# Kernel optimization log

Hardware: AMD Instinct MI355X
Metric: run time of the kernel (lower is better)

Reference implementation:

```python
import jax, jax.numpy as jnp
import numpy as np

# ---- model constants (match init_kwargs) ----
E = 128; GH = 8; GD = E // GH; GL = 3          # graph emb / heads / layers
SH = 4; SD = E // SH; SL = 4                   # sequence transformer
ATOM = 64; BOND = 16; RBF_K = 32; CUTOFF = 5.0
VOCAB = 64; SEQL = 128
N = 32                                          # nodes per graph (equal-size graphs)
GC = 64; GS = 16; BMOL = 16; DEG = 64; GF = 3   # conf graphs / scaffold graphs / molecules / edges-per-graph
LN_EPS = 1e-5
CENTERS = jnp.linspace(0.0, CUTOFF, RBF_K)
GAMMA = (CUTOFF / (RBF_K - 1)) ** -2            # GaussianRBF gamma = (center spacing)^-2


def _ln(x, g, b):
    mu = x.mean(-1, keepdims=True)
    var = ((x - mu) ** 2).mean(-1, keepdims=True)
    return (x - mu) / jnp.sqrt(var + LN_EPS) * g + b


def _graph_encoder(x, edge_index, edge_attr, pos, G, p):
    # node projection
    h = x @ p["gproj_w"] + p["gproj_b"]                      # [G*N, E]
    # edge features: bond features + RBF(distance)
    d = jnp.clip(edge_attr[:, -1], 0.0, 10.0)
    rbf = jnp.exp(-GAMMA * (d[:, None] - CENTERS) ** 2)       # [M, K]
    ef = jnp.concatenate([edge_attr[:, :-1], rbf], axis=1)    # [M, BOND+K]
    # EdgeNetwork: per-edge matrix (gather -> matvec -> scatter-add)
    M = ef.shape[0]
    m = (ef @ p["elin_w"] + p["elin_b"]).reshape(M, E, E)
    msg = jnp.einsum("mef,mf->me", m, h[edge_index[1]])      # [M, E]
    aggr = jnp.zeros_like(h).at[edge_index[0]].add(msg)
    h = _ln(h + aggr, p["eln_g"], p["eln_b"])
    # dense per-graph layout (equal-size graphs -> reshape, mask is all-true)
    hb = h.reshape(G, N, E)
    pp = pos.reshape(G, N, 3)
    d2 = jnp.sum((pp[:, :, None, :] - pp[:, None, :, :]) ** 2, axis=-1)
    dist = jnp.where(d2 > 0, jnp.sqrt(jnp.where(d2 > 0, d2, 1.0)), 0.0)  # safe cdist
    inv_sqrt_d = 1.0 / np.sqrt(GD)
    for l in range(GL):
        def heads(t):
            return t.reshape(G, N, GH, GD).transpose(0, 2, 1, 3)
        q = heads(hb @ p["gt_qw"][l] + p["gt_qb"][l])
        k = heads(hb @ p["gt_kw"][l] + p["gt_kb"][l])
        v = heads(hb @ p["gt_vw"][l] + p["gt_vb"][l])
        s = jnp.einsum("bhnd,bhmd->bhnm", q, k) * inv_sqrt_d + dist[:, None]
        s = jnp.clip(s, -10.0, 10.0)
        a = jax.nn.softmax(s, axis=-1)                       # all nodes valid -> no mask
        o = jnp.einsum("bhnm,bhmd->bhnd", a, v).transpose(0, 2, 1, 3).reshape(G, N, E)
        o = o @ p["gt_ow"][l] + p["gt_ob"][l]
        x1 = _ln(hb + o, p["gt_ln1g"][l], p["gt_ln1b"][l])
        ff = jax.nn.relu(x1 @ p["gt_f1w"][l] + p["gt_f1b"][l]) @ p["gt_f2w"][l] + p["gt_f2b"][l]
        hb = _ln(x1 + ff, p["gt_ln2g"][l], p["gt_ln2b"][l])
    # masked mean pool with the source's eps in the denominator
    return hb.sum(1) / (N + 1e-8)


def _seq_encoder(tokens, p):
    B, L = tokens.shape
    x = p["tok_emb"][tokens] + p["pos_emb"][:L][None]        # [B, L, E]
    inv_sqrt_d = 1.0 / np.sqrt(SD)
    for l in range(SL):
        qkv = x @ p["se_inw"][l] + p["se_inb"][l]            # [B, L, 3E]
        q, k, v = jnp.split(qkv, 3, axis=-1)
        def heads(t):
            return t.reshape(B, L, SH, SD).transpose(0, 2, 1, 3)
        q, k, v = heads(q), heads(k), heads(v)
        a = jax.nn.softmax(jnp.einsum("bhnd,bhmd->bhnm", q, k) * inv_sqrt_d, axis=-1)
        o = jnp.einsum("bhnm,bhmd->bhnd", a, v).transpose(0, 2, 1, 3).reshape(B, L, E)
        o = o @ p["se_ow"][l] + p["se_ob"][l]
        x = _ln(x + o, p["se_ln1g"][l], p["se_ln1b"][l])      # post-norm (torch default)
        ff = jax.nn.relu(x @ p["se_f1w"][l] + p["se_f1b"][l]) @ p["se_f2w"][l] + p["se_f2b"][l]
        x = _ln(x + ff, p["se_ln2g"][l], p["se_ln2b"][l])
    return x.mean(1)                                          # [B, E]


def _forward(p, conf_edge_index, scaf_edge_index, tokens, conf_per_mol):
    g_all = _graph_encoder(p["conf_x"], conf_edge_index, p["conf_edge_attr"], p["conf_pos"], GC, p)
    conf_emb = g_all.reshape(-1, conf_per_mol, E).mean(1)     # per-molecule conformer mean (equal counts)
    scaf_emb = _graph_encoder(p["scaf_x"], scaf_edge_index, p["scaf_edge_attr"], p["scaf_pos"], GS, p)
    total = conf_emb + scaf_emb
    seq = _seq_encoder(tokens, p)
    # FusionGating
    gate_h = jax.nn.relu(jnp.concatenate([total, seq], -1) @ p["fg1_w"] + p["fg1_b"])
    gate = jax.nn.sigmoid(gate_h @ p["fg2_w"] + p["fg2_b"])
    fused = gate * total + (1.0 - gate) * seq
    # CrossModalAttention: MHA over a length-1 sequence (unsqueeze(0)) -> softmax
    # weights are identically 1, so attn(q_in, kv, kv) == out_proj(v_proj(kv)).
    g, s = fused, fused
    for l in range(2):
        g2s = (s @ p["cm_g2s_vw"][l] + p["cm_g2s_vb"][l]) @ p["cm_g2s_ow"][l] + p["cm_g2s_ob"][l]
        g = _ln(g + g2s, p["cm_n1g"][l], p["cm_n1b"][l])
        s2g = (g @ p["cm_s2g_vw"][l] + p["cm_s2g_vb"][l]) @ p["cm_s2g_ow"][l] + p["cm_s2g_ob"][l]
        s = _ln(s + s2g, p["cm_n2g"][l], p["cm_n2b"][l])
    final = (g + s) * 0.5
    comb = jnp.concatenate([final, p["graph_features"]], -1)
    return (jax.nn.relu(comb @ p["r1_w"] + p["r1_b"]) @ p["r2_w"] + p["r2_b"])[:, 0]


def setup_inputs() -> dict:
    ks = iter(jax.random.split(jax.random.key(0), 64))
    def nrm(shape, s):
        return (jax.random.normal(next(ks), shape) * s).astype(jnp.float32)
    inp = {}
    def mk_graph(prefix, G):
        inp[prefix + "_x"] = nrm((G * N, ATOM), 1.0)
        off = (jnp.arange(G) * N)[:, None]
        src = jax.random.randint(next(ks), (G, DEG), 0, N) + off   # within-graph edges
        dst = jax.random.randint(next(ks), (G, DEG), 0, N) + off
        inp[prefix + "_edge_index"] = jnp.stack([src.ravel(), dst.ravel()]).astype(jnp.int32)
        bond = jax.random.uniform(next(ks), (G * DEG, BOND))
        dist = jax.random.uniform(next(ks), (G * DEG, 1), minval=0.5, maxval=CUTOFF)
        inp[prefix + "_edge_attr"] = jnp.concatenate([bond, dist], 1).astype(jnp.float32)
        inp[prefix + "_pos"] = nrm((G * N, 3), 2.0)
    mk_graph("conf", GC)
    mk_graph("scaf", GS)
    inp["tokens"] = jax.random.randint(next(ks), (BMOL, SEQL), 1, VOCAB).astype(jnp.int32)
    inp["graph_features"] = nrm((BMOL, GF), 1.0)
    inp["conf_per_mol"] = GC // BMOL
    W = 0.05
    inp["gproj_w"] = nrm((ATOM, E), W); inp["gproj_b"] = jnp.zeros(E)
    inp["elin_w"] = nrm((BOND + RBF_K, E * E), W); inp["elin_b"] = jnp.zeros(E * E)
    inp["eln_g"] = jnp.ones(E); inp["eln_b"] = jnp.zeros(E)
    for nm in ["qw", "kw", "vw", "ow"]:
        inp["gt_" + nm] = nrm((GL, E, E), W)
        inp["gt_" + nm[0] + "b"] = jnp.zeros((GL, E))
    inp["gt_ln1g"] = jnp.ones((GL, E)); inp["gt_ln1b"] = jnp.zeros((GL, E))
    inp["gt_f1w"] = nrm((GL, E, 2 * E), W); inp["gt_f1b"] = jnp.zeros((GL, 2 * E))
    inp["gt_f2w"] = nrm((GL, 2 * E, E), W); inp["gt_f2b"] = jnp.zeros((GL, E))
    inp["gt_ln2g"] = jnp.ones((GL, E)); inp["gt_ln2b"] = jnp.zeros((GL, E))
    inp["tok_emb"] = nrm((VOCAB, E), 0.02); inp["pos_emb"] = nrm((256, E), 0.02)
    inp["se_inw"] = nrm((SL, E, 3 * E), W); inp["se_inb"] = jnp.zeros((SL, 3 * E))
    inp["se_ow"] = nrm((SL, E, E), W); inp["se_ob"] = jnp.zeros((SL, E))
    inp["se_ln1g"] = jnp.ones((SL, E)); inp["se_ln1b"] = jnp.zeros((SL, E))
    inp["se_f1w"] = nrm((SL, E, 2 * E), W); inp["se_f1b"] = jnp.zeros((SL, 2 * E))
    inp["se_f2w"] = nrm((SL, 2 * E, E), W); inp["se_f2b"] = jnp.zeros((SL, E))
    inp["se_ln2g"] = jnp.ones((SL, E)); inp["se_ln2b"] = jnp.zeros((SL, E))
    inp["fg1_w"] = nrm((2 * E, 64), W); inp["fg1_b"] = jnp.zeros(64)
    inp["fg2_w"] = nrm((64, E), W); inp["fg2_b"] = jnp.zeros(E)
    for nm in ["g2s", "s2g"]:
        inp["cm_" + nm + "_vw"] = nrm((2, E, E), W); inp["cm_" + nm + "_vb"] = jnp.zeros((2, E))
        inp["cm_" + nm + "_ow"] = nrm((2, E, E), W); inp["cm_" + nm + "_ob"] = jnp.zeros((2, E))
    inp["cm_n1g"] = jnp.ones((2, E)); inp["cm_n1b"] = jnp.zeros((2, E))
    inp["cm_n2g"] = jnp.ones((2, E)); inp["cm_n2b"] = jnp.zeros((2, E))
    inp["r1_w"] = nrm((E + GF, E), W); inp["r1_b"] = jnp.zeros(E)
    inp["r2_w"] = nrm((E, 1), W); inp["r2_b"] = jnp.zeros(1)
    return inp


def reference(conf_x, conf_edge_attr, conf_pos, scaf_x, scaf_edge_attr, scaf_pos, graph_features,
              gproj_w, gproj_b, elin_w, elin_b, eln_g, eln_b,
              gt_qw, gt_qb, gt_kw, gt_kb, gt_vw, gt_vb, gt_ow, gt_ob,
              gt_ln1g, gt_ln1b, gt_f1w, gt_f1b, gt_f2w, gt_f2b, gt_ln2g, gt_ln2b,
              tok_emb, pos_emb,
              se_inw, se_inb, se_ow, se_ob, se_ln1g, se_ln1b, se_f1w, se_f1b, se_f2w, se_f2b, se_ln2g, se_ln2b,
              fg1_w, fg1_b, fg2_w, fg2_b,
              cm_g2s_vw, cm_g2s_vb, cm_g2s_ow, cm_g2s_ob, cm_n1g, cm_n1b,
              cm_s2g_vw, cm_s2g_vb, cm_s2g_ow, cm_s2g_ob, cm_n2g, cm_n2b,
              r1_w, r1_b, r2_w, r2_b,
              conf_edge_index, scaf_edge_index, tokens, conf_per_mol):
    p = dict(locals())
    return _forward(p, conf_edge_index, scaf_edge_index, tokens, conf_per_mol)
```

## Files before the change

### kernel.cpp

```cpp
#include <hip/hip_runtime.h>
#include <hip/hip_bf16.h>


__device__ __forceinline__ float blk_norm(float v, int e, float* sred)
{
  float s = v;
  #pragma unroll
  for (int o = 1; o < 64; o <<= 1) s += __shfl_xor(s, o);
  if ((e & 63) == 0) sred[e >> 6] = s;
  __syncthreads();
  float mean = (sred[0] + sred[1]) * (1.0f / 128.0f);
  __syncthreads();
  float d = v - mean;
  float s2 = d * d;
  #pragma unroll
  for (int o = 1; o < 64; o <<= 1) s2 += __shfl_xor(s2, o);
  if ((e & 63) == 0) sred[e >> 6] = s2;
  __syncthreads();
  float var = (sred[0] + sred[1]) * (1.0f / 128.0f);
  __syncthreads();
  return d / sqrtf(var + 1e-5f);
}

__global__ __launch_bounds__(128) void node_proj_k(
    const float* __restrict__ cx, const float* __restrict__ sx,
    const float* __restrict__ w, const float* __restrict__ b,
    float* __restrict__ h, float* __restrict__ aggr)
{
  int r = blockIdx.x, e = threadIdx.x;
  const float* x = (r < 2048) ? (cx + (size_t)r * 64) : (sx + (size_t)(r - 2048) * 64);
  __shared__ float xs[64];
  if (e < 64) xs[e] = x[e];
  __syncthreads();
  float acc = b[e];
  for (int a = 0; a < 64; a++) acc += xs[a] * w[a * 128 + e];
  h[(size_t)r * 128 + e] = acc;
  aggr[(size_t)r * 128 + e] = 0.0f;
}

__global__ __launch_bounds__(256) void dist_k(
    const float* __restrict__ cpos, const float* __restrict__ spos, float* __restrict__ dist)
{
  int g = blockIdx.x, tid = threadIdx.x;
  __shared__ float P[96];
  const float* p = (g < 64) ? (cpos + (size_t)g * 96) : (spos + (size_t)(g - 64) * 96);
  if (tid < 96) P[tid] = p[tid];
  __syncthreads();
  #pragma unroll
  for (int jj = 0; jj < 4; jj++) {
    int idx = tid * 4 + jj;
    int i = idx >> 5, j = idx & 31;
    float dx = P[i * 3 + 0] - P[j * 3 + 0];
    float dy = P[i * 3 + 1] - P[j * 3 + 1];
    float dz = P[i * 3 + 2] - P[j * 3 + 2];
    float d2 = dx * dx + dy * dy + dz * dz;
    dist[(size_t)g * 1024 + idx] = (d2 > 0.0f) ? sqrtf(d2) : 0.0f;
  }
}

__global__ __launch_bounds__(256) void edge_gemm_k(
    const float* __restrict__ cea, const float* __restrict__ sea,
    const int* __restrict__ cei, const int* __restrict__ sei,
    const float* __restrict__ h,
    const float* __restrict__ elw, const float* __restrict__ elb,
    float* __restrict__ aggr)
{
  __shared__ float efs[32][8];
  __shared__ float As[32][36];
  __shared__ float Bs[32][136];
  const int tid = threadIdx.x;
  const int m0 = blockIdx.x * 32;
  const int kt0 = blockIdx.y * 28;
  const int c0 = kt0 >> 2;
  {
    int t = tid >> 3, cc = tid & 7;
    if (cc < 7) {
      int c = c0 + cc;
      int m = m0 + t;
      const float* attr = (m < 4096) ? (cea + (size_t)m * 17) : (sea + (size_t)(m - 4096) * 17);
      float val;
      if (c < 16) val = attr[c];
      else if (c < 48) {
        float d = fminf(fmaxf(attr[16], 0.0f), 10.0f);
        float t2 = d - (float)((c - 16) * (5.0 / 31.0));
        val = expf(-38.44f * t2 * t2);
      } else val = 1.0f;
      efs[t][cc] = val;
    }
  }
  const int gk = tid & 31, gt = (tid >> 5) * 4;
  float hreg[4][4];
  #pragma unroll
  for (int i = 0; i < 4; i++) {
    int m = m0 + gt + i;
    int dst = (m < 4096) ? cei[4096 + m] : (sei[1024 + (m - 4096)] + 2048);
    const float* hp = h + (size_t)dst * 128 + gk;
    hreg[i][0] = hp[0]; hreg[i][1] = hp[32]; hreg[i][2] = hp[64]; hreg[i][3] = hp[96];
  }
  const int tn = tid & 31, tm = tid >> 5;
  const int e0 = 4 * tn, t0 = 4 * tm;
  const int se = tid >> 1, sk = (tid & 1) * 16;
  float acc[4][4] = {};
  __syncthreads();
  #pragma unroll 1
  for (int kt = kt0; kt < kt0 + 28; kt++) {
    int c = kt >> 2, cc = c - c0, j = kt & 3;
    float4 av;
    av.x = efs[gt + 0][cc] * hreg[0][j];
    av.y = efs[gt + 1][cc] * hreg[1][j];
    av.z = efs[gt + 2][cc] * hreg[2][j];
    av.w = efs[gt + 3][cc] * hreg[3][j];
    *(float4*)&As[gk][gt] = av;
    const float* bp = ((c < 48) ? (elw + (size_t)c * 16384) : elb) + (size_t)se * 128 + j * 32 + sk;
    float4 w0 = *(const float4*)(bp + 0);
    float4 w1 = *(const float4*)(bp + 4);
    float4 w2 = *(const float4*)(bp + 8);
    float4 w3 = *(const float4*)(bp + 12);
    Bs[sk + 0][se] = w0.x;  Bs[sk + 1][se] = w0.y;  Bs[sk + 2][se] = w0.z;  Bs[sk + 3][se] = w0.w;
    Bs[sk + 4][se] = w1.x;  Bs[sk + 5][se] = w1.y;  Bs[sk + 6][se] = w1.z;  Bs[sk + 7][se] = w1.w;
    Bs[sk + 8][se] = w2.x;  Bs[sk + 9][se] = w2.y;  Bs[sk + 10][se] = w2.z; Bs[sk + 11][se] = w2.w;
    Bs[sk + 12][se] = w3.x; Bs[sk + 13][se] = w3.y; Bs[sk + 14][se] = w3.z; Bs[sk + 15][se] = w3.w;
    __syncthreads();
    #pragma unroll
    for (int kk = 0; kk < 32; kk++) {
      float4 a = *(const float4*)&As[kk][t0];
      float4 b = *(const float4*)&Bs[kk][e0];
      acc[0][0] += a.x * b.x; acc[0][1] += a.x * b.y; acc[0][2] += a.x * b.z; acc[0][3] += a.x * b.w;
      acc[1][0] += a.y * b.x; acc[1][1] += a.y * b.y; acc[1][2] += a.y * b.z; acc[1][3] += a.y * b.w;
      acc[2][0] += a.z * b.x; acc[2][1] += a.z * b.y; acc[2][2] += a.z * b.z; acc[2][3] += a.z * b.w;
      acc[3][0] += a.w * b.x; acc[3][1] += a.w * b.y; acc[3][2] += a.w * b.z; acc[3][3] += a.w * b.w;
    }
    __syncthreads();
  }
  #pragma unroll
  for (int i = 0; i < 4; i++) {
    int m = m0 + t0 + i;
    int src = (m < 4096) ? cei[m] : (sei[m - 4096] + 2048);
    float* dst = aggr + (size_t)src * 128 + e0;
    atomicAdd(dst + 0, acc[i][0]);
    atomicAdd(dst + 1, acc[i][1]);
    atomicAdd(dst + 2, acc[i][2]);
    atomicAdd(dst + 3, acc[i][3]);
  }
}

__device__ __forceinline__ void gemm16_body(
    const float* __restrict__ A, const float* __restrict__ Bp,
    const float* __restrict__ biasp, float* __restrict__ Cp,
    int row0, int ldb, int ldc)
{
  __shared__ float Sa[32][20];
  __shared__ float Bs[32][136];
  const int tid = threadIdx.x;
  const int tm = tid >> 5, tn = tid & 31;
  const int t0 = 2 * tm, e0 = 4 * tn;
  const int ar = tid >> 4, ak = (tid & 15) * 2;
  const int bk = tid >> 3, be = (tid & 7) * 16;
  float acc[2][4] = {};
  for (int k0 = 0; k0 < 128; k0 += 32) {
    float2 av = *(const float2*)(A + (size_t)(row0 + ar) * 128 + k0 + ak);
    Sa[ak][ar] = av.x; Sa[ak + 1][ar] = av.y;
    const float* bp = Bp + (size_t)(k0 + bk) * ldb + be;
    float4 b0v = *(const float4*)(bp + 0);
    float4 b1v = *(const float4*)(bp + 4);
    float4 b2v = *(const float4*)(bp + 8);
    float4 b3v = *(const float4*)(bp + 12);
    Bs[bk][be + 0] = b0v.x;  Bs[bk][be + 1] = b0v.y;  Bs[bk][be + 2] = b0v.z;  Bs[bk][be + 3] = b0v.w;
    Bs[bk][be + 4] = b1v.x;  Bs[bk][be + 5] = b1v.y;  Bs[bk][be + 6] = b1v.z;  Bs[bk][be + 7] = b1v.w;
    Bs[bk][be + 8] = b2v.x;  Bs[bk][be + 9] = b2v.y;  Bs[bk][be + 10] = b2v.z; Bs[bk][be + 11] = b2v.w;
    Bs[bk][be + 12] = b3v.x; Bs[bk][be + 13] = b3v.y; Bs[bk][be + 14] = b3v.z; Bs[bk][be + 15] = b3v.w;
    __syncthreads();
    #pragma unroll
    for (int kk = 0; kk < 32; kk++) {
      float2 a = *(const float2*)&Sa[kk][t0];
      float4 b = *(const float4*)&Bs[kk][e0];
      acc[0][0] += a.x * b.x; acc[0][1] += a.x * b.y; acc[0][2] += a.x * b.z; acc[0][3] += a.x * b.w;
      acc[1][0] += a.y * b.x; acc[1][1] += a.y * b.y; acc[1][2] += a.y * b.z; acc[1][3] += a.y * b.w;
    }
    __syncthreads();
  }
  #pragma unroll
  for (int i = 0; i < 2; i++) {
    float* cp = Cp + (size_t)(row0 + t0 + i) * ldc + e0;
    #pragma unroll
    for (int j = 0; j < 4; j++) cp[j] = acc[i][j] + biasp[e0 + j];
  }
}

__global__ __launch_bounds__(256) void qkv_k(
    int gBlocks,
    const float* __restrict__ ghb,
    const float* gqw, const float* gkw, const float* gvw,
    const float* gqb, const float* gkb, const float* gvb, float* gout,
    const float* __restrict__ sxs, const float* sw, const float* sb, float* sout)
{
  int bx = blockIdx.x;
  if (bx < gBlocks) {
    int z = bx / 160, rt = bx % 160;
    const float* B = (z == 0) ? gqw : (z == 1) ? gkw : gvw;
    const float* bias = (z == 0) ? gqb : (z == 1) ? gkb : gvb;
    gemm16_body(ghb, B, bias, gout + (size_t)z * 327680, rt * 16, 128, 128);
  } else {
    int i = bx - gBlocks;
    int z = i >> 7, rt = i & 127;
    gemm16_body(sxs, sw + z * 128, sb + z * 128, sout + z * 128, rt * 16, 384, 384);
  }
}

__device__ __forceinline__ void gattn_body(
    int g, int h, const float* __restrict__ q, const float* __restrict__ k,
    const float* __restrict__ v, const float* __restrict__ dist, float* __restrict__ o)
{
  __shared__ float qs[32][17], ksh[32][17], vsh[32][17], ss[32][33], rs[32];
  const int tid = threadIdx.x;
  {
    int idx = tid * 2;
    int i = idx >> 4, d = idx & 15;
    size_t base = ((size_t)(g * 32 + i)) * 128 + h * 16 + d;
    qs[i][d] = q[base];  qs[i][d + 1] = q[base + 1];
    ksh[i][d] = k[base]; ksh[i][d + 1] = k[base + 1];
    vsh[i][d] = v[base]; vsh[i][d + 1] = v[base + 1];
  }
  __syncthreads();
  {
    int i = tid >> 3, j0 = (tid & 7) * 4;
    for (int j = j0; j < j0 + 4; j++) {
      float a = 0;
      #pragma unroll
      for (int d = 0; d < 16; d++) a += qs[i][d] * ksh[j][d];
      a = a * 0.25f + dist[(size_t)g * 1024 + i * 32 + j];
      ss[i][j] = fminf(fmaxf(a, -10.0f), 10.0f);
    }
  }
  __syncthreads();
  if (tid < 32) {
    float m = -1e30f;
    for (int j = 0; j < 32; j++) m = fmaxf(m, ss[tid][j]);
    float sm = 0;
    for (int j = 0; j < 32; j++) { float ex = expf(ss[tid][j] - m); ss[tid][j] = ex; sm += ex; }
    rs[tid] = 1.0f / sm;
  }
  __syncthreads();
  {
    int idx = tid * 2;
    int i = idx >> 4, d = idx & 15;
    float a0 = 0, a1 = 0;
    for (int j = 0; j < 32; j++) { float wj = ss[i][j]; a0 += wj * vsh[j][d]; a1 += wj * vsh[j][d + 1]; }
    float r = rs[i];
    size_t base = ((size_t)(g * 32 + i)) * 128 + h * 16 + d;
    o[base] = a0 * r; o[base + 1] = a1 * r;
  }
}

__device__ __forceinline__ void sattn_body(
    int b, int h, int qt, const float* __restrict__ qkv, float* __restrict__ o)
{
  __shared__ float ks[128][33];
  __shared__ float vs[128][33];
  __shared__ float qs2[32][33];
  __shared__ float ss2[32][129];
  __shared__ float red[32][8];
  __shared__ float red2[32][8];
  const int tid = threadIdx.x;
  {
    int l = tid >> 1, d0 = (tid & 1) * 16;
    const float* kp = qkv + ((size_t)(b * 128 + l)) * 384 + 128 + h * 32 + d0;
    #pragma unroll
    for (int j = 0; j < 16; j++) { ks[l][d0 + j] = kp[j]; vs[l][d0 + j] = kp[128 + j]; }
  }
  {
    int i = tid >> 3, d0 = (tid & 7) * 4;
    const float* qp = qkv + ((size_t)(b * 128 + qt * 32 + i)) * 384 + h * 32 + d0;
    #pragma unroll
    for (int j = 0; j < 4; j++) qs2[i][d0 + j] = qp[j];
  }
  __syncthreads();
  const int i = tid >> 3, sub = tid & 7;
  {
    int j0 = sub * 16;
    for (int j = j0; j < j0 + 16; j++) {
      float a = 0;
      #pragma unroll
      for (int d = 0; d < 32; d++) a += qs2[i][d] * ks[j][d];
      ss2[i][j] = a * 0.17677669529663687f;
    }
  }
  __syncthreads();
  float m = -1e30f;
  for (int j = sub; j < 128; j += 8) m = fmaxf(m, ss2[i][j]);
  red[i][sub] = m;
  __syncthreads();
  float mm = red[i][0];
  #pragma unroll
  for (int t = 1; t < 8; t++) mm = fmaxf(mm, red[i][t]);
  float ps = 0;
  for (int j = sub; j < 128; j += 8) { float ex = expf(ss2[i][j] - mm); ss2[i][j] = ex; ps += ex; }
  red2[i][sub] = ps;
  __syncthreads();
  float sm = 0;
  #pragma unroll
  for (int t = 0; t < 8; t++) sm += red2[i][t];
  float rinv = 1.0f / sm;
  {
    int d0 = sub * 4;
    float a0 = 0, a1 = 0, a2 = 0, a3 = 0;
    for (int j = 0; j < 128; j++) {
      float wj = ss2[i][j];
      a0 += wj * vs[j][d0 + 0]; a1 += wj * vs[j][d0 + 1];
      a2 += wj * vs[j][d0 + 2]; a3 += wj * vs[j][d0 + 3];
    }
    float* op = o + ((size_t)(b * 128 + qt * 32 + i)) * 128 + h * 32 + d0;
    op[0] = a0 * rinv; op[1] = a1 * rinv; op[2] = a2 * rinv; op[3] = a3 * rinv;
  }
}

__global__ __launch_bounds__(256) void attn_k(
    int gBlocks, const float* q, const float* k, const float* v,
    const float* dist, float* go, const float* qkv, float* so)
{
  int bx = blockIdx.x;
  if (bx < gBlocks) gattn_body(bx >> 3, bx & 7, q, k, v, dist, go);
  else { int i = bx - gBlocks; sattn_body(i >> 4, (i >> 2) & 3, i & 3, qkv, so); }
}

__device__ __forceinline__ void tail_body(
    int row0, const float* __restrict__ A,
    const float* __restrict__ Wo, const float* __restrict__ bo, const float* __restrict__ res,
    const float* __restrict__ g1, const float* __restrict__ b1n,
    const float* __restrict__ W1, const float* __restrict__ b1f,
    const float* __restrict__ W2, const float* __restrict__ b2f,
    const float* __restrict__ g2, const float* __restrict__ b2n,
    float* __restrict__ Out)
{
  __shared__ float x1[16][132];
  __shared__ float hid[16][260];
  __shared__ __align__(16) float sbuf[4352];
  __shared__ float Sa[32][20];
  float (*BsA)[136] = (float(*)[136])sbuf;
  float (*Bs1)[260] = (float(*)[260])sbuf;
  float (*Bs2)[136] = (float(*)[136])sbuf;
  const int tid = threadIdx.x;
  {
    const int tm = tid >> 5, tn = tid & 31;
    const int t0 = 2 * tm, e0 = 4 * tn;
    const int ar = tid >> 4, ak = (tid & 15) * 2;
    const int bk = tid >> 3, be = (tid & 7) * 16;
    float acc[2][4] = {};
    for (int k0 = 0; k0 < 128; k0 += 32) {
      float2 av = *(const float2*)(A + (size_t)(row0 + ar) * 128 + k0 + ak);
      Sa[ak][ar] = av.x; Sa[ak + 1][ar] = av.y;
      const float* bp = Wo + (size_t)(k0 + bk) * 128 + be;
      float4 b0v = *(const float4*)(bp + 0);
      float4 b1v = *(const float4*)(bp + 4);
      float4 b2v = *(const float4*)(bp + 8);
      float4 b3v = *(const float4*)(bp + 12);
      BsA[bk][be + 0] = b0v.x;  BsA[bk][be + 1] = b0v.y;  BsA[bk][be + 2] = b0v.z;  BsA[bk][be + 3] = b0v.w;
      BsA[bk][be + 4] = b1v.x;  BsA[bk][be + 5] = b1v.y;  BsA[bk][be + 6] = b1v.z;  BsA[bk][be + 7] = b1v.w;
      BsA[bk][be + 8] = b2v.x;  BsA[bk][be + 9] = b2v.y;  BsA[bk][be + 10] = b2v.z; BsA[bk][be + 11] = b2v.w;
      BsA[bk][be + 12] = b3v.x; BsA[bk][be + 13] = b3v.y; BsA[bk][be + 14] = b3v.z; BsA[bk][be + 15] = b3v.w;
      __syncthreads();
      #pragma unroll
      for (int kk = 0; kk < 32; kk++) {
        float2 a = *(const float2*)&Sa[kk][t0];
        float4 b = *(const float4*)&BsA[kk][e0];
        acc[0][0] += a.x * b.x; acc[0][1] += a.x * b.y; acc[0][2] += a.x * b.z; acc[0][3] += a.x * b.w;
        acc[1][0] += a.y * b.x; acc[1][1] += a.y * b.y; acc[1][2] += a.y * b.z; acc[1][3] += a.y * b.w;
      }
      __syncthreads();
    }
    #pragma unroll
    for (int i = 0; i < 2; i++) {
      int r = row0 + t0 + i;
      float v0 = acc[i][0] + bo[e0 + 0] + res[(size_t)r * 128 + e0 + 0];
      float v1 = acc[i][1] + bo[e0 + 1] + res[(size_t)r * 128 + e0 + 1];
      float v2 = acc[i][2] + bo[e0 + 2] + res[(size_t)r * 128 + e0 + 2];
      float v3 = acc[i][3] + bo[e0 + 3] + res[(size_t)r * 128 + e0 + 3];
      float s = v0 + v1 + v2 + v3;
      #pragma unroll
      for (int o = 1; o < 32; o <<= 1) s += __shfl_xor(s, o);
      float mean = s * (1.0f / 128.0f);
      float d0 = v0 - mean, d1 = v1 - mean, d2 = v2 - mean, d3 = v3 - mean;
      float sq = d0 * d0 + d1 * d1 + d2 * d2 + d3 * d3;
      #pragma unroll
      for (int o = 1; o < 32; o <<= 1) sq += __shfl_xor(sq, o);
      float rstd = 1.0f / sqrtf(sq * (1.0f / 128.0f) + 1e-5f);
      x1[t0 + i][e0 + 0] = d0 * rstd * g1[e0 + 0] + b1n[e0 + 0];
      x1[t0 + i][e0 + 1] = d1 * rstd * g1[e0 + 1] + b1n[e0 + 1];
      x1[t0 + i][e0 + 2] = d2 * rstd * g1[e0 + 2] + b1n[e0 + 2];
      x1[t0 + i][e0 + 3] = d3 * rstd * g1[e0 + 3] + b1n[e0 + 3];
    }
  }
  __syncthreads();
  {
    const int tm = tid >> 6, tn = tid & 63;
    const int t0 = 4 * tm, e0 = 4 * tn;
    const int ar = tid >> 4, ak = tid & 15;
    const int bk = tid >> 4, be = (tid & 15) * 16;
    float acc[4][4] = {};
    for (int k0 = 0; k0 < 128; k0 += 16) {
      Sa[ak][ar] = x1[ar][k0 + ak];
      const float* bp = W1 + (size_t)(k0 + bk) * 256 + be;
      float4 b0v = *(const float4*)(bp + 0);
      float4 b1v = *(const float4*)(bp + 4);
      float4 b2v = *(const float4*)(bp + 8);
      float4 b3v = *(const float4*)(bp + 12);
      Bs1[bk][be + 0] = b0v.x;  Bs1[bk][be + 1] = b0v.y;  Bs1[bk][be + 2] = b0v.z;  Bs1[bk][be + 3] = b0v.w;
      Bs1[bk][be + 4] = b1v.x;  Bs1[bk][be + 5] = b1v.y;  Bs1[bk][be + 6] = b1v.z;  Bs1[bk][be + 7] = b1v.w;
      Bs1[bk][be + 8] = b2v.x;  Bs1[bk][be + 9] = b2v.y;  Bs1[bk][be + 10] = b2v.z; Bs1[bk][be + 11] = b2v.w;
      Bs1[bk][be + 12] = b3v.x; Bs1[bk][be + 13] = b3v.y; Bs1[bk][be + 14] = b3v.z; Bs1[bk][be + 15] = b3v.w;
      __syncthreads();
      #pragma unroll
      for (int kk = 0; kk < 16; kk++) {
        float4 a = *(const float4*)&Sa[kk][t0];
        float4 b = *(const float4*)&Bs1[kk][e0];
        acc[0][0] += a.x * b.x; acc[0][1] += a.x * b.y; acc[0][2] += a.x * b.z; acc[0][3] += a.x * b.w;
        acc[1][0] += a.y * b.x; acc[1][1] += a.y * b.y; acc[1][2] += a.y * b.z; acc[1][3] += a.y * b.w;
        acc[2][0] += a.z * b.x; acc[2][1] += a.z * b.y; acc[2][2] += a.z * b.z; acc[2][3] += a.z * b.w;
        acc[3][0] += a.w * b.x; acc[3][1] += a.w * b.y; acc[3][2] += a.w * b.z; acc[3][3] += a.w * b.w;
      }
      __syncthreads();
    }
    #pragma unroll
    for (int i = 0; i < 4; i++) {
      float4 hv;
      hv.x = fmaxf(acc[i][0] + b1f[e0 + 0], 0.0f);
      hv.y = fmaxf(acc[i][1] + b1f[e0 + 1], 0.0f);
      hv.z = fmaxf(acc[i][2] + b1f[e0 + 2], 0.0f);
      hv.w = fmaxf(acc[i][3] + b1f[e0 + 3], 0.0f);
      *(float4*)&hid[t0 + i][e0] = hv;
    }
  }
  __syncthreads();
  {
    const int tm = tid >> 5, tn = tid & 31;
    const int t0 = 2 * tm, e0 = 4 * tn;
    const int bk = tid >> 3, be = (tid & 7) * 16;
    float acc[2][4] = {};
    for (int k0 = 0; k0 < 256; k0 += 32) {
      const float* bp = W2 + (size_t)(k0 + bk) * 128 + be;
      float4 b0v = *(const float4*)(bp + 0);
      float4 b1v = *(const float4*)(bp + 4);
      float4 b2v = *(const float4*)(bp + 8);
      float4 b3v = *(const float4*)(bp + 12);
      Bs2[bk][be + 0] = b0v.x;  Bs2[bk][be + 1] = b0v.y;  Bs2[bk][be + 2] = b0v.z;  Bs2[bk][be + 3] = b0v.w;
      Bs2[bk][be + 4] = b1v.x;  Bs2[bk][be + 5] = b1v.y;  Bs2[bk][be + 6] = b1v.z;  Bs2[bk][be + 7] = b1v.w;
      Bs2[bk][be + 8] = b2v.x;  Bs2[bk][be + 9] = b2v.y;  Bs2[bk][be + 10] = b2v.z; Bs2[bk][be + 11] = b2v.w;
      Bs2[bk][be + 12] = b3v.x; Bs2[bk][be + 13] = b3v.y; Bs2[bk][be + 14] = b3v.z; Bs2[bk][be + 15] = b3v.w;
      __syncthreads();
      #pragma unroll
      for (int kk = 0; kk < 32; kk++) {
        float a0 = hid[t0 + 0][k0 + kk];
        float a1 = hid[t0 + 1][k0 + kk];
        float4 b = *(const float4*)&Bs2[kk][e0];
        acc[0][0] += a0 * b.x; acc[0][1] += a0 * b.y; acc[0][2] += a0 * b.z; acc[0][3] += a0 * b.w;
        acc[1][0] += a1 * b.x; acc[1][1] += a1 * b.y; acc[1][2] += a1 * b.z; acc[1][3] += a1 * b.w;
      }
      __syncthreads();
    }
    #pragma unroll
    for (int i = 0; i < 2; i++) {
      int r = row0 + t0 + i;
      float v0 = acc[i][0] + b2f[e0 + 0] + x1[t0 + i][e0 + 0];
      float v1 = acc[i][1] + b2f[e0 + 1] + x1[t0 + i][e0 + 1];
      float v2 = acc[i][2] + b2f[e0 + 2] + x1[t0 + i][e0 + 2];
      float v3 = acc[i][3] + b2f[e0 + 3] + x1[t0 + i][e0 + 3];
      float s = v0 + v1 + v2 + v3;
      #pragma unroll
      for (int o = 1; o < 32; o <<= 1) s += __shfl_xor(s, o);
      float mean = s * (1.0f / 128.0f);
      float d0 = v0 - mean, d1 = v1 - mean, d2 = v2 - mean, d3 = v3 - mean;
      float sq = d0 * d0 + d1 * d1 + d2 * d2 + d3 * d3;
      #pragma unroll
      for (int o = 1; o < 32; o <<= 1) sq += __shfl_xor(sq, o);
      float rstd = 1.0f / sqrtf(sq * (1.0f / 128.0f) + 1e-5f);
      float* cp = Out + (size_t)r * 128 + e0;
      cp[0] = d0 * rstd * g2[e0 + 0] + b2n[e0 + 0];
      cp[1] = d1 * rstd * g2[e0 + 1] + b2n[e0 + 1];
      cp[2] = d2 * rstd * g2[e0 + 2] + b2n[e0 + 2];
      cp[3] = d3 * rstd * g2[e0 + 3] + b2n[e0 + 3];
    }
  }
}

__global__ __launch_bounds__(256) void tail_k(
    int gBlocks,
    const float* gA, const float* gWo, const float* gbo, const float* gres,
    const float* gg1, const float* gb1, const float* gW1, const float* gbf1,
    const float* gW2, const float* gbf2, const float* gg2, const float* gb2, float* gOut,
    const float* sA, const float* sWo, const float* sbo, const float* sres,
    const float* sg1, const float* sb1, const float* sW1, const float* sbf1,
    const float* sW2, const float* sbf2, const float* sg2, const float* sb2, float* sOut)
{
  int bx = blockIdx.x;
  if (bx < gBlocks)
    tail_body(bx * 16, gA, gWo, gbo, gres, gg1, gb1, gW1, gbf1, gW2, gbf2, gg2, gb2, gOut);
  else
    tail_body((bx - gBlocks) * 16, sA, sWo, sbo, sres, sg1, sb1, sW1, sbf1, sW2, sbf2, sg2, sb2, sOut);
}

__global__ __launch_bounds__(128) void ln_k(
    const float* __restrict__ x, const float* __restrict__ res,
    const float* __restrict__ g, const float* __restrict__ b, float* __restrict__ out)
{
  __shared__ float sred[2];
  int r = blockIdx.x, e = threadIdx.x;
  size_t idx = (size_t)r * 128 + e;
  float v = x[idx] + res[idx];
  float nv = blk_norm(v, e, sred);
  out[idx] = nv * g[e] + b[e];
}

__global__ __launch_bounds__(128) void embed_k(
    const int* __restrict__ tokens, const float* __restrict__ tok_emb,
    const float* __restrict__ pos_emb, float* __restrict__ xs)
{
  int r = blockIdx.x, e = threadIdx.x;
  int tk = tokens[r];
  xs[(size_t)r * 128 + e] = tok_emb[(size_t)tk * 128 + e] + pos_emb[(size_t)(r & 127) * 128 + e];
}

__global__ __launch_bounds__(128) void head_k(
    const float* __restrict__ hb, const float* __restrict__ xs, const float* __restrict__ gfeat,
    const float* fg1w, const float* fg1b, const float* fg2w, const float* fg2b,
    const float* g2s_vw, const float* g2s_vb, const float* g2s_ow, const float* g2s_ob,
    const float* n1g, const float* n1b,
    const float* s2g_vw, const float* s2g_vb, const float* s2g_ow, const float* s2g_ob,
    const float* n2g, const float* n2b,
    const float* r1w, const float* r1b, const float* r2w, const float* r2b,
    float* __restrict__ out)
{
  __shared__ float T[128], S[128], G[128], Sm[128], t1[128], t2[128], gh[64], sred[2];
  int mol = blockIdx.x, e = threadIdx.x;
  {
    float cs = 0;
    for (int c = 0; c < 4; c++) {
      int g = mol * 4 + c;
      float s = 0;
      for (int i = 0; i < 32; i++) s += hb[((size_t)(g * 32 + i)) * 128 + e];
      cs += s * (1.0f / 32.0f);
    }
    cs *= 0.25f;
    float s2 = 0;
    int g = 64 + mol;
    for (int i = 0; i < 32; i++) s2 += hb[((size_t)(g * 32 + i)) * 128 + e];
    T[e] = cs + s2 * (1.0f / 32.0f);
    float ss = 0;
    for (int l = 0; l < 128; l++) ss += xs[((size_t)(mol * 128 + l)) * 128 + e];
    S[e] = ss * (1.0f / 128.0f);
  }
  __syncthreads();
  if (e < 64) {
    float a = fg1b[e];
    for (int f = 0; f < 128; f++) a += T[f] * fg1w[f * 64 + e];
    for (int f = 0; f < 128; f++) a += S[f] * fg1w[(128 + f) * 64 + e];
    gh[e] = fmaxf(a, 0.0f);
  }
  __syncthreads();
  {
    float a = fg2b[e];
    for (int j = 0; j < 64; j++) a += gh[j] * fg2w[j * 128 + e];
    float gate = 1.0f / (1.0f + expf(-a));
    float fu = gate * T[e] + (1.0f - gate) * S[e];
    G[e] = fu; Sm[e] = fu;
  }
  __syncthreads();
  for (int l = 0; l < 2; l++) {
    const float* vw = g2s_vw + (size_t)l * 16384; const float* vb = g2s_vb + l * 128;
    const float* ow = g2s_ow + (size_t)l * 16384; const float* ob = g2s_ob + l * 128;
    float a = vb[e];
    for (int f = 0; f < 128; f++) a += Sm[f] * vw[f * 128 + e];
    t1[e] = a;
    __syncthreads();
    a = ob[e];
    for (int f = 0; f < 128; f++) a += t1[f] * ow[f * 128 + e];
    float nv = blk_norm(G[e] + a, e, sred);
    G[e] = nv * n1g[l * 128 + e] + n1b[l * 128 + e];
    __syncthreads();
    const float* vw2 = s2g_vw + (size_t)l * 16384; const float* vb2 = s2g_vb + l * 128;
    const float* ow2 = s2g_ow + (size_t)l * 16384; const float* ob2 = s2g_ob + l * 128;
    a = vb2[e];
    for (int f = 0; f < 128; f++) a += G[f] * vw2[f * 128 + e];
    t1[e] = a;
    __syncthreads();
    a = ob2[e];
    for (int f = 0; f < 128; f++) a += t1[f] * ow2[f * 128 + e];
    nv = blk_norm(Sm[e] + a, e, sred);
    Sm[e] = nv * n2g[l * 128 + e] + n2b[l * 128 + e];
    __syncthreads();
  }
  t2[e] = 0.5f * (G[e] + Sm[e]);
  __syncthreads();
  float a = r1b[e];
  for (int f = 0; f < 128; f++) a += t2[f] * r1w[f * 128 + e];
  for (int f = 0; f < 3; f++) a += gfeat[mol * 3 + f] * r1w[(128 + f) * 128 + e];
  a = fmaxf(a, 0.0f);
  float p = a * r2w[e];
  #pragma unroll
  for (int o = 1; o < 64; o <<= 1) p += __shfl_xor(p, o);
  if ((e & 63) == 0) sred[e >> 6] = p;
  __syncthreads();
  if (e == 0) out[mol] = sred[0] + sred[1] + r2b[0];
}

extern "C" void kernel_launch(void* const* d_in, const int* in_sizes, int n_in,
                              void* d_out, int out_size, void* d_ws, size_t ws_size,
                              hipStream_t stream)
{
  (void)n_in; (void)out_size; (void)ws_size;
  const bool dict = (in_sizes[1] == 8192);
  auto IN = [&](int di, int si) { return d_in[dict ? di : si]; };

  const float* conf_x   = (const float*)IN(0, 0);
  const int*   conf_ei  = (const int*)  IN(1, 63);
  const float* conf_ea  = (const float*)IN(2, 1);
  const float* conf_pos = (const float*)IN(3, 2);
  const float* scaf_x   = (const float*)IN(4, 3);
  const int*   scaf_ei  = (const int*)  IN(5, 64);
  const float* scaf_ea  = (const float*)IN(6, 4);
  const float* scaf_pos = (const float*)IN(7, 5);
  const int*   tokens   = (const int*)  IN(8, 65);
  const float* gfeat    = (const float*)IN(9, 6);
  const float* gproj_w  = (const float*)IN(11, 7);
  const float* gproj_b  = (const float*)IN(12, 8);
  const float* elin_w   = (const float*)IN(13, 9);
  const float* elin_b   = (const float*)IN(14, 10);
  const float* eln_g    = (const float*)IN(15, 11);
  const float* eln_b    = (const float*)IN(16, 12);
  const float* gt_qw    = (const float*)IN(17, 13);
  const float* gt_qb    = (const float*)IN(18, 14);
  const float* gt_kw    = (const float*)IN(19, 15);
  const float* gt_kb    = (const float*)IN(20, 16);
  const float* gt_vw    = (const float*)IN(21, 17);
  const float* gt_vb    = (const float*)IN(22, 18);
  const float* gt_ow    = (const float*)IN(23, 19);
  const float* gt_ob    = (const float*)IN(24, 20);
  const float* gt_ln1g  = (const float*)IN(25, 21);
  const float* gt_ln1b  = (const float*)IN(26, 22);
  const float* gt_f1w   = (const float*)IN(27, 23);
  const float* gt_f1b   = (const float*)IN(28, 24);
  const float* gt_f2w   = (const float*)IN(29, 25);
  const float* gt_f2b   = (const float*)IN(30, 26);
  const float* gt_ln2g  = (const float*)IN(31, 27);
  const float* gt_ln2b  = (const float*)IN(32, 28);
  const float* tok_emb  = (const float*)IN(33, 29);
  const float* pos_emb  = (const float*)IN(34, 30);
  const float* se_inw   = (const float*)IN(35, 31);
  const float* se_inb   = (const float*)IN(36, 32);
  const float* se_ow    = (const float*)IN(37, 33);
  const float* se_ob    = (const float*)IN(38, 34);
  const float* se_ln1g  = (const float*)IN(39, 35);
  const float* se_ln1b  = (const float*)IN(40, 36);
  const float* se_f1w   = (const float*)IN(41, 37);
  const float* se_f1b   = (const float*)IN(42, 38);
  const float* se_f2w   = (const float*)IN(43, 39);
  const float* se_f2b   = (const float*)IN(44, 40);
  const float* se_ln2g  = (const float*)IN(45, 41);
  const float* se_ln2b  = (const float*)IN(46, 42);
  const float* fg1_w    = (const float*)IN(47, 43);
  const float* fg1_b    = (const float*)IN(48, 44);
  const float* fg2_w    = (const float*)IN(49, 45);
  const float* fg2_b    = (const float*)IN(50, 46);
  const float* cm_g2s_vw = (const float*)IN(51, 47);
  const float* cm_g2s_vb = (const float*)IN(52, 48);
  const float* cm_g2s_ow = (const float*)IN(53, 49);
  const float* cm_g2s_ob = (const float*)IN(54, 50);
  const float* cm_s2g_vw = (const float*)IN(55, 53);
  const float* cm_s2g_vb = (const float*)IN(56, 54);
  const float* cm_s2g_ow = (const float*)IN(57, 55);
  const float* cm_s2g_ob = (const float*)IN(58, 56);
  const float* cm_n1g   = (const float*)IN(59, 51);
  const float* cm_n1b   = (const float*)IN(60, 52);
  const float* cm_n2g   = (const float*)IN(61, 57);
  const float* cm_n2b   = (const float*)IN(62, 58);
  const float* r1_w     = (const float*)IN(63, 59);
  const float* r1_b     = (const float*)IN(64, 60);
  const float* r2_w     = (const float*)IN(65, 61);
  const float* r2_b     = (const float*)IN(66, 62);
  float* out = (float*)d_out;

  float* w = (float*)d_ws;
  size_t off = 0;
  auto alloc = [&](size_t n) { float* p = w + off; off += n; return p; };
  float* h     = alloc(2560 * 128);
  float* aggr  = alloc(2560 * 128);
  float* hb    = alloc(2560 * 128);
  float* distb = alloc(80 * 1024);
  float* qb    = alloc(3 * 327680);
  float* atto  = alloc(327680);
  float* xs2   = alloc(2048 * 128);
  float* qkv3  = alloc(2048 * 384);
  float* satto = alloc(2048 * 128);
  float* xsfin = alloc(2048 * 128);

  node_proj_k<<<2560, 128, 0, stream>>>(conf_x, scaf_x, gproj_w, gproj_b, h, aggr);
  dist_k<<<80, 256, 0, stream>>>(conf_pos, scaf_pos, distb);
  edge_gemm_k<<<dim3(160, 7), 256, 0, stream>>>(conf_ea, scaf_ea, conf_ei, scaf_ei, h, elin_w, elin_b, aggr);
  ln_k<<<2560, 128, 0, stream>>>(aggr, h, eln_g, eln_b, hb);
  embed_k<<<2048, 128, 0, stream>>>(tokens, tok_emb, pos_emb, xs2);

  for (int l = 0; l < 4; l++) {
    const bool hasG = (l < 3);
    const int lg = hasG ? l : 0;
    const int gq = hasG ? 480 : 0;
    const int ga = hasG ? 640 : 0;
    const int gt = hasG ? 160 : 0;
    float* sOut = (l == 3) ? xsfin : xs2;
    qkv_k<<<gq + 384, 256, 0, stream>>>(gq,
        hb, gt_qw + (size_t)lg * 16384, gt_kw + (size_t)lg * 16384, gt_vw + (size_t)lg * 16384,
        gt_qb + lg * 128, gt_kb + lg * 128, gt_vb + lg * 128, qb,
        xs2, se_inw + (size_t)l * 49152, se_inb + l * 384, qkv3);
    attn_k<<<ga + 256, 256, 0, stream>>>(ga, qb, qb + 327680, qb + 655360, distb, atto, qkv3, satto);
    tail_k<<<gt + 128, 256, 0, stream>>>(gt,
        atto, gt_ow + (size_t)lg * 16384, gt_ob + lg * 128, hb,
        gt_ln1g + lg * 128, gt_ln1b + lg * 128,
        gt_f1w + (size_t)lg * 32768, gt_f1b + lg * 256,
        gt_f2w + (size_t)lg * 32768, gt_f2b + lg * 128,
        gt_ln2g + lg * 128, gt_ln2b + lg * 128, hb,
        satto, se_ow + (size_t)l * 16384, se_ob + l * 128, xs2,
        se_ln1g + l * 128, se_ln1b + l * 128,
        se_f1w + (size_t)l * 32768, se_f1b + l * 256,
        se_f2w + (size_t)l * 32768, se_f2b + l * 128,
        se_ln2g + l * 128, se_ln2b + l * 128, sOut);
  }

  head_k<<<16, 128, 0, stream>>>(hb, xsfin, gfeat,
                                 fg1_w, fg1_b, fg2_w, fg2_b,
                                 cm_g2s_vw, cm_g2s_vb, cm_g2s_ow, cm_g2s_ob, cm_n1g, cm_n1b,
                                 cm_s2g_vw, cm_s2g_vb, cm_s2g_ow, cm_s2g_ob, cm_n2g, cm_n2b,
                                 r1_w, r1_b, r2_w, r2_b, out);
}
```

Before: 663.6 us.

## Skew graph and sequence branches across fused kernels to cut launch count

Graph-transformer and sequence-transformer stages are re-paired so each launch runs one graph stage alongside a different sequence stage, offset by one phase. For example, the edge GEMM now shares a launch with the sequence QKV, and the LayerNorm with sequence attention. Node projection, distance and embedding are merged into a single front kernel, and shared memory is overlaid through unions. This reduces the number of launches and the serialisation between the two independent branches, but makes the per-block shared-memory footprint equal to the largest branch, which may lower occupancy.

```diff
diff --git a/kernel.cpp b/kernel.cpp
--- a/kernel.cpp
+++ b/kernel.cpp
@@ -2,75 +2,70 @@
 #include <hip/hip_bf16.h>
 
 
-__device__ __forceinline__ float blk_norm(float v, int e, float* sred)
-{
-  float s = v;
-  #pragma unroll
-  for (int o = 1; o < 64; o <<= 1) s += __shfl_xor(s, o);
-  if ((e & 63) == 0) sred[e >> 6] = s;
-  __syncthreads();
-  float mean = (sred[0] + sred[1]) * (1.0f / 128.0f);
-  __syncthreads();
-  float d = v - mean;
-  float s2 = d * d;
-  #pragma unroll
-  for (int o = 1; o < 64; o <<= 1) s2 += __shfl_xor(s2, o);
-  if ((e & 63) == 0) sred[e >> 6] = s2;
-  __syncthreads();
-  float var = (sred[0] + sred[1]) * (1.0f / 128.0f);
-  __syncthreads();
-  return d / sqrtf(var + 1e-5f);
-}
-
-__global__ __launch_bounds__(128) void node_proj_k(
+struct __align__(16) EdgeSm  { float efs[32][8]; float As[32][36]; float Bs[32][136]; };
+struct __align__(16) G16Sm   { float Sa[32][20]; float Bs[32][136]; };
+struct __align__(16) GAttnSm { float qs[32][17], ksh[32][17], vsh[32][17], ss[32][33], rs[32]; };
+struct __align__(16) SAttnSm { float ks[128][33], vs[128][33], qs2[32][33], ss2[32][129], red[32][8], red2[32][8]; };
+struct __align__(16) TailSm  { float x1[16][132]; float hid[16][260]; float sbuf[4352]; float Sa[32][20]; };
+
+union K1U { EdgeSm e; G16Sm g; };
+union K2U { float sred4[4]; SAttnSm s; };
+union K3U { G16Sm g; TailSm t; };
+union K4U { GAttnSm a; G16Sm g; };
+union K5U { TailSm t; SAttnSm s; };
+
+__global__ __launch_bounds__(256) void front_k(
     const float* __restrict__ cx, const float* __restrict__ sx,
     const float* __restrict__ w, const float* __restrict__ b,
-    float* __restrict__ h, float* __restrict__ aggr)
-{
-  int r = blockIdx.x, e = threadIdx.x;
-  const float* x = (r < 2048) ? (cx + (size_t)r * 64) : (sx + (size_t)(r - 2048) * 64);
-  __shared__ float xs[64];
-  if (e < 64) xs[e] = x[e];
-  __syncthreads();
-  float acc = b[e];
-  for (int a = 0; a < 64; a++) acc += xs[a] * w[a * 128 + e];
-  h[(size_t)r * 128 + e] = acc;
-  aggr[(size_t)r * 128 + e] = 0.0f;
-}
-
-__global__ __launch_bounds__(256) void dist_k(
-    const float* __restrict__ cpos, const float* __restrict__ spos, float* __restrict__ dist)
-{
-  int g = blockIdx.x, tid = threadIdx.x;
-  __shared__ float P[96];
-  const float* p = (g < 64) ? (cpos + (size_t)g * 96) : (spos + (size_t)(g - 64) * 96);
-  if (tid < 96) P[tid] = p[tid];
-  __syncthreads();
-  #pragma unroll
-  for (int jj = 0; jj < 4; jj++) {
-    int idx = tid * 4 + jj;
-    int i = idx >> 5, j = idx & 31;
-    float dx = P[i * 3 + 0] - P[j * 3 + 0];
-    float dy = P[i * 3 + 1] - P[j * 3 + 1];
-    float dz = P[i * 3 + 2] - P[j * 3 + 2];
-    float d2 = dx * dx + dy * dy + dz * dz;
-    dist[(size_t)g * 1024 + idx] = (d2 > 0.0f) ? sqrtf(d2) : 0.0f;
-  }
-}
-
-__global__ __launch_bounds__(256) void edge_gemm_k(
+    float* __restrict__ h, float* __restrict__ aggr,
+    const float* __restrict__ cpos, const float* __restrict__ spos, float* __restrict__ dist,
+    const int* __restrict__ tokens, const float* __restrict__ tok_emb,
+    const float* __restrict__ pos_emb, float* __restrict__ xs)
+{
+  __shared__ float sP[128];
+  const int bx = blockIdx.x, tid = threadIdx.x;
+  if (bx < 1280) {
+    int r = bx * 2 + (tid >> 7), e = tid & 127;
+    const float* x = (r < 2048) ? (cx + (size_t)r * 64) : (sx + (size_t)(r - 2048) * 64);
+    float* xrow = sP + (tid >> 7) * 64;
+    if (e < 64) xrow[e] = x[e];
+    __syncthreads();
+    float acc = b[e];
+    for (int a = 0; a < 64; a++) acc += xrow[a] * w[a * 128 + e];
+    h[(size_t)r * 128 + e] = acc;
+    aggr[(size_t)r * 128 + e] = 0.0f;
+  } else if (bx < 1360) {
+    int g = bx - 1280;
+    const float* p = (g < 64) ? (cpos + (size_t)g * 96) : (spos + (size_t)(g - 64) * 96);
+    if (tid < 96) sP[tid] = p[tid];
+    __syncthreads();
+    #pragma unroll
+    for (int jj = 0; jj < 4; jj++) {
+      int idx = tid * 4 + jj;
+      int i = idx >> 5, j = idx & 31;
+      float dx = sP[i * 3 + 0] - sP[j * 3 + 0];
+      float dy = sP[i * 3 + 1] - sP[j * 3 + 1];
+      float dz = sP[i * 3 + 2] - sP[j * 3 + 2];
+      float d2 = dx * dx + dy * dy + dz * dz;
+      dist[(size_t)g * 1024 + idx] = (d2 > 0.0f) ? sqrtf(d2) : 0.0f;
+    }
+  } else {
+    int r = (bx - 1360) * 2 + (tid >> 7), e = tid & 127;
+    int tk = tokens[r];
+    xs[(size_t)r * 128 + e] = tok_emb[(size_t)tk * 128 + e] + pos_emb[(size_t)(r & 127) * 128 + e];
+  }
+}
+
+__device__ __forceinline__ void edge_body(EdgeSm& sm, int eb,
     const float* __restrict__ cea, const float* __restrict__ sea,
     const int* __restrict__ cei, const int* __restrict__ sei,
     const float* __restrict__ h,
     const float* __restrict__ elw, const float* __restrict__ elb,
     float* __restrict__ aggr)
 {
-  __shared__ float efs[32][8];
-  __shared__ float As[32][36];
-  __shared__ float Bs[32][136];
   const int tid = threadIdx.x;
-  const int m0 = blockIdx.x * 32;
-  const int kt0 = blockIdx.y * 28;
+  const int m0 = (eb % 160) * 32;
+  const int kt0 = (eb / 160) * 28;
   const int c0 = kt0 >> 2;
   {
     int t = tid >> 3, cc = tid & 7;
@@ -85,7 +80,7 @@
         float t2 = d - (float)((c - 16) * (5.0 / 31.0));
         val = expf(-38.44f * t2 * t2);
       } else val = 1.0f;
-      efs[t][cc] = val;
+      sm.efs[t][cc] = val;
     }
   }
   const int gk = tid & 31, gt = (tid >> 5) * 4;
@@ -106,25 +101,25 @@
   for (int kt = kt0; kt < kt0 + 28; kt++) {
     int c = kt >> 2, cc = c - c0, j = kt & 3;
     float4 av;
-    av.x = efs[gt + 0][cc] * hreg[0][j];
-    av.y = efs[gt + 1][cc] * hreg[1][j];
-    av.z = efs[gt + 2][cc] * hreg[2][j];
-    av.w = efs[gt + 3][cc] * hreg[3][j];
-    *(float4*)&As[gk][gt] = av;
+    av.x = sm.efs[gt + 0][cc] * hreg[0][j];
+    av.y = sm.efs[gt + 1][cc] * hreg[1][j];
+    av.z = sm.efs[gt + 2][cc] * hreg[2][j];
+    av.w = sm.efs[gt + 3][cc] * hreg[3][j];
+    *(float4*)&sm.As[gk][gt] = av;
     const float* bp = ((c < 48) ? (elw + (size_t)c * 16384) : elb) + (size_t)se * 128 + j * 32 + sk;
     float4 w0 = *(const float4*)(bp + 0);
     float4 w1 = *(const float4*)(bp + 4);
     float4 w2 = *(const float4*)(bp + 8);
     float4 w3 = *(const float4*)(bp + 12);
-    Bs[sk + 0][se] = w0.x;  Bs[sk + 1][se] = w0.y;  Bs[sk + 2][se] = w0.z;  Bs[sk + 3][se] = w0.w;
-    Bs[sk + 4][se] = w1.x;  Bs[sk + 5][se] = w1.y;  Bs[sk + 6][se] = w1.z;  Bs[sk + 7][se] = w1.w;
-    Bs[sk + 8][se] = w2.x;  Bs[sk + 9][se] = w2.y;  Bs[sk + 10][se] = w2.z; Bs[sk + 11][se] = w2.w;
-    Bs[sk + 12][se] = w3.x; Bs[sk + 13][se] = w3.y; Bs[sk + 14][se] = w3.z; Bs[sk + 15][se] = w3.w;
+    sm.Bs[sk + 0][se] = w0.x;  sm.Bs[sk + 1][se] = w0.y;  sm.Bs[sk + 2][se] = w0.z;  sm.Bs[sk + 3][se] = w0.w;
+    sm.Bs[sk + 4][se] = w1.x;  sm.Bs[sk + 5][se] = w1.y;  sm.Bs[sk + 6][se] = w1.z;  sm.Bs[sk + 7][se] = w1.w;
+    sm.Bs[sk + 8][se] = w2.x;  sm.Bs[sk + 9][se] = w2.y;  sm.Bs[sk + 10][se] = w2.z; sm.Bs[sk + 11][se] = w2.w;
+    sm.Bs[sk + 12][se] = w3.x; sm.Bs[sk + 13][se] = w3.y; sm.Bs[sk + 14][se] = w3.z; sm.Bs[sk + 15][se] = w3.w;
     __syncthreads();
     #pragma unroll
     for (int kk = 0; kk < 32; kk++) {
-      float4 a = *(const float4*)&As[kk][t0];
-      float4 b = *(const float4*)&Bs[kk][e0];
+      float4 a = *(const float4*)&sm.As[kk][t0];
+      float4 b = *(const float4*)&sm.Bs[kk][e0];
       acc[0][0] += a.x * b.x; acc[0][1] += a.x * b.y; acc[0][2] += a.x * b.z; acc[0][3] += a.x * b.w;
       acc[1][0] += a.y * b.x; acc[1][1] += a.y * b.y; acc[1][2] += a.y * b.z; acc[1][3] += a.y * b.w;
       acc[2][0] += a.z * b.x; acc[2][1] += a.z * b.y; acc[2][2] += a.z * b.z; acc[2][3] += a.z * b.w;
@@ -144,13 +139,11 @@
   }
 }
 
-__device__ __forceinline__ void gemm16_body(
+__device__ __forceinline__ void gemm16_body(G16Sm& sm,
     const float* __restrict__ A, const float* __restrict__ Bp,
     const float* __restrict__ biasp, float* __restrict__ Cp,
     int row0, int ldb, int ldc)
 {
-  __shared__ float Sa[32][20];
-  __shared__ float Bs[32][136];
   const int tid = threadIdx.x;
   const int tm = tid >> 5, tn = tid & 31;
   const int t0 = 2 * tm, e0 = 4 * tn;
@@ -159,21 +152,21 @@
   float acc[2][4] = {};
   for (int k0 = 0; k0 < 128; k0 += 32) {
     float2 av = *(const float2*)(A + (size_t)(row0 + ar) * 128 + k0 + ak);
-    Sa[ak][ar] = av.x; Sa[ak + 1][ar] = av.y;
+    sm.Sa[ak][ar] = av.x; sm.Sa[ak + 1][ar] = av.y;
     const float* bp = Bp + (size_t)(k0 + bk) * ldb + be;
     float4 b0v = *(const float4*)(bp + 0);
     float4 b1v = *(const float4*)(bp + 4);
     float4 b2v = *(const float4*)(bp + 8);
     float4 b3v = *(const float4*)(bp + 12);
-    Bs[bk][be + 0] = b0v.x;  Bs[bk][be + 1] = b0v.y;  Bs[bk][be + 2] = b0v.z;  Bs[bk][be + 3] = b0v.w;
-    Bs[bk][be + 4] = b1v.x;  Bs[bk][be + 5] = b1v.y;  Bs[bk][be + 6] = b1v.z;  Bs[bk][be + 7] = b1v.w;
-    Bs[bk][be + 8] = b2v.x;  Bs[bk][be + 9] = b2v.y;  Bs[bk][be + 10] = b2v.z; Bs[bk][be + 11] = b2v.w;
-    Bs[bk][be + 12] = b3v.x; Bs[bk][be + 13] = b3v.y; Bs[bk][be + 14] = b3v.z; Bs[bk][be + 15] = b3v.w;
+    sm.Bs[bk][be + 0] = b0v.x;  sm.Bs[bk][be + 1] = b0v.y;  sm.Bs[bk][be + 2] = b0v.z;  sm.Bs[bk][be + 3] = b0v.w;
+    sm.Bs[bk][be + 4] = b1v.x;  sm.Bs[bk][be + 5] = b1v.y;  sm.Bs[bk][be + 6] = b1v.z;  sm.Bs[bk][be + 7] = b1v.w;
+    sm.Bs[bk][be + 8] = b2v.x;  sm.Bs[bk][be + 9] = b2v.y;  sm.Bs[bk][be + 10] = b2v.z; sm.Bs[bk][be + 11] = b2v.w;
+    sm.Bs[bk][be + 12] = b3v.x; sm.Bs[bk][be + 13] = b3v.y; sm.Bs[bk][be + 14] = b3v.z; sm.Bs[bk][be + 15] = b3v.w;
     __syncthreads();
     #pragma unroll
     for (int kk = 0; kk < 32; kk++) {
-      float2 a = *(const float2*)&Sa[kk][t0];
-      float4 b = *(const float4*)&Bs[kk][e0];
+      float2 a = *(const float2*)&sm.Sa[kk][t0];
+      float4 b = *(const float4*)&sm.Bs[kk][e0];
       acc[0][0] += a.x * b.x; acc[0][1] += a.x * b.y; acc[0][2] += a.x * b.z; acc[0][3] += a.x * b.w;
       acc[1][0] += a.y * b.x; acc[1][1] += a.y * b.y; acc[1][2] += a.y * b.z; acc[1][3] += a.y * b.w;
     }
@@ -187,39 +180,18 @@
   }
 }
 
-__global__ __launch_bounds__(256) void qkv_k(
-    int gBlocks,
-    const float* __restrict__ ghb,
-    const float* gqw, const float* gkw, const float* gvw,
-    const float* gqb, const float* gkb, const float* gvb, float* gout,
-    const float* __restrict__ sxs, const float* sw, const float* sb, float* sout)
-{
-  int bx = blockIdx.x;
-  if (bx < gBlocks) {
-    int z = bx / 160, rt = bx % 160;
-    const float* B = (z == 0) ? gqw : (z == 1) ? gkw : gvw;
-    const float* bias = (z == 0) ? gqb : (z == 1) ? gkb : gvb;
-    gemm16_body(ghb, B, bias, gout + (size_t)z * 327680, rt * 16, 128, 128);
-  } else {
-    int i = bx - gBlocks;
-    int z = i >> 7, rt = i & 127;
-    gemm16_body(sxs, sw + z * 128, sb + z * 128, sout + z * 128, rt * 16, 384, 384);
-  }
-}
-
-__device__ __forceinline__ void gattn_body(
-    int g, int h, const float* __restrict__ q, const float* __restrict__ k,
+__device__ __forceinline__ void gattn_body(GAttnSm& sm, int g, int h,
+    const float* __restrict__ q, const float* __restrict__ k,
     const float* __restrict__ v, const float* __restrict__ dist, float* __restrict__ o)
 {
-  __shared__ float qs[32][17], ksh[32][17], vsh[32][17], ss[32][33], rs[32];
   const int tid = threadIdx.x;
   {
     int idx = tid * 2;
     int i = idx >> 4, d = idx & 15;
     size_t base = ((size_t)(g * 32 + i)) * 128 + h * 16 + d;
-    qs[i][d] = q[base];  qs[i][d + 1] = q[base + 1];
-    ksh[i][d] = k[base]; ksh[i][d + 1] = k[base + 1];
-    vsh[i][d] = v[base]; vsh[i][d + 1] = v[base + 1];
+    sm.qs[i][d] = q[base];  sm.qs[i][d + 1] = q[base + 1];
+    sm.ksh[i][d] = k[base]; sm.ksh[i][d + 1] = k[base + 1];
+    sm.vsh[i][d] = v[base]; sm.vsh[i][d + 1] = v[base + 1];
   }
   __syncthreads();
   {
@@ -227,52 +199,46 @@
     for (int j = j0; j < j0 + 4; j++) {
       float a = 0;
       #pragma unroll
-      for (int d = 0; d < 16; d++) a += qs[i][d] * ksh[j][d];
+      for (int d = 0; d < 16; d++) a += sm.qs[i][d] * sm.ksh[j][d];
       a = a * 0.25f + dist[(size_t)g * 1024 + i * 32 + j];
-      ss[i][j] = fminf(fmaxf(a, -10.0f), 10.0f);
+      sm.ss[i][j] = fminf(fmaxf(a, -10.0f), 10.0f);
     }
   }
   __syncthreads();
   if (tid < 32) {
     float m = -1e30f;
-    for (int j = 0; j < 32; j++) m = fmaxf(m, ss[tid][j]);
-    float sm = 0;
-    for (int j = 0; j < 32; j++) { float ex = expf(ss[tid][j] - m); ss[tid][j] = ex; sm += ex; }
-    rs[tid] = 1.0f / sm;
+    for (int j = 0; j < 32; j++) m = fmaxf(m, sm.ss[tid][j]);
+    float s = 0;
+    for (int j = 0; j < 32; j++) { float ex = expf(sm.ss[tid][j] - m); sm.ss[tid][j] = ex; s += ex; }
+    sm.rs[tid] = 1.0f / s;
   }
   __syncthreads();
   {
     int idx = tid * 2;
     int i = idx >> 4, d = idx & 15;
     float a0 = 0, a1 = 0;
-    for (int j = 0; j < 32; j++) { float wj = ss[i][j]; a0 += wj * vsh[j][d]; a1 += wj * vsh[j][d + 1]; }
-    float r = rs[i];
+    for (int j = 0; j < 32; j++) { float wj = sm.ss[i][j]; a0 += wj * sm.vsh[j][d]; a1 += wj * sm.vsh[j][d + 1]; }
+    float r = sm.rs[i];
     size_t base = ((size_t)(g * 32 + i)) * 128 + h * 16 + d;
     o[base] = a0 * r; o[base + 1] = a1 * r;
   }
 }
 
-__device__ __forceinline__ void sattn_body(
-    int b, int h, int qt, const float* __restrict__ qkv, float* __restrict__ o)
-{
-  __shared__ float ks[128][33];
-  __shared__ float vs[128][33];
-  __shared__ float qs2[32][33];
-  __shared__ float ss2[32][129];
-  __shared__ float red[32][8];
-  __shared__ float red2[32][8];
+__device__ __forceinline__ void sattn_body(SAttnSm& sm, int b, int h, int qt,
+    const float* __restrict__ qkv, float* __restrict__ o)
+{
   const int tid = threadIdx.x;
   {
     int l = tid >> 1, d0 = (tid & 1) * 16;
     const float* kp = qkv + ((size_t)(b * 128 + l)) * 384 + 128 + h * 32 + d0;
     #pragma unroll
-    for (int j = 0; j < 16; j++) { ks[l][d0 + j] = kp[j]; vs[l][d0 + j] = kp[128 + j]; }
+    for (int j = 0; j < 16; j++) { sm.ks[l][d0 + j] = kp[j]; sm.vs[l][d0 + j] = kp[128 + j]; }
   }
   {
     int i = tid >> 3, d0 = (tid & 7) * 4;
     const float* qp = qkv + ((size_t)(b * 128 + qt * 32 + i)) * 384 + h * 32 + d0;
     #pragma unroll
-    for (int j = 0; j < 4; j++) qs2[i][d0 + j] = qp[j];
+    for (int j = 0; j < 4; j++) sm.qs2[i][d0 + j] = qp[j];
   }
   __syncthreads();
   const int i = tid >> 3, sub = tid & 7;
@@ -281,50 +247,40 @@
     for (int j = j0; j < j0 + 16; j++) {
       float a = 0;
       #pragma unroll
-      for (int d = 0; d < 32; d++) a += qs2[i][d] * ks[j][d];
-      ss2[i][j] = a * 0.17677669529663687f;
+      for (int d = 0; d < 32; d++) a += sm.qs2[i][d] * sm.ks[j][d];
+      sm.ss2[i][j] = a * 0.17677669529663687f;
     }
   }
   __syncthreads();
   float m = -1e30f;
-  for (int j = sub; j < 128; j += 8) m = fmaxf(m, ss2[i][j]);
-  red[i][sub] = m;
-  __syncthreads();
-  float mm = red[i][0];
+  for (int j = sub; j < 128; j += 8) m = fmaxf(m, sm.ss2[i][j]);
+  sm.red[i][sub] = m;
+  __syncthreads();
+  float mm = sm.red[i][0];
   #pragma unroll
-  for (int t = 1; t < 8; t++) mm = fmaxf(mm, red[i][t]);
+  for (int t = 1; t < 8; t++) mm = fmaxf(mm, sm.red[i][t]);
   float ps = 0;
-  for (int j = sub; j < 128; j += 8) { float ex = expf(ss2[i][j] - mm); ss2[i][j] = ex; ps += ex; }
-  red2[i][sub] = ps;
-  __syncthreads();
-  float sm = 0;
+  for (int j = sub; j < 128; j += 8) { float ex = expf(sm.ss2[i][j] - mm); sm.ss2[i][j] = ex; ps += ex; }
+  sm.red2[i][sub] = ps;
+  __syncthreads();
+  float s = 0;
   #pragma unroll
-  for (int t = 0; t < 8; t++) sm += red2[i][t];
-  float rinv = 1.0f / sm;
+  for (int t = 0; t < 8; t++) s += sm.red2[i][t];
+  float rinv = 1.0f / s;
   {
     int d0 = sub * 4;
     float a0 = 0, a1 = 0, a2 = 0, a3 = 0;
     for (int j = 0; j < 128; j++) {
-      float wj = ss2[i][j];
-      a0 += wj * vs[j][d0 + 0]; a1 += wj * vs[j][d0 + 1];
-      a2 += wj * vs[j][d0 + 2]; a3 += wj * vs[j][d0 + 3];
+      float wj = sm.ss2[i][j];
+      a0 += wj * sm.vs[j][d0 + 0]; a1 += wj * sm.vs[j][d0 + 1];
+      a2 += wj * sm.vs[j][d0 + 2]; a3 += wj * sm.vs[j][d0 + 3];
     }
     float* op = o + ((size_t)(b * 128 + qt * 32 + i)) * 128 + h * 32 + d0;
     op[0] = a0 * rinv; op[1] = a1 * rinv; op[2] = a2 * rinv; op[3] = a3 * rinv;
   }
 }
 
-__global__ __launch_bounds__(256) void attn_k(
-    int gBlocks, const float* q, const float* k, const float* v,
-    const float* dist, float* go, const float* qkv, float* so)
-{
-  int bx = blockIdx.x;
-  if (bx < gBlocks) gattn_body(bx >> 3, bx & 7, q, k, v, dist, go);
-  else { int i = bx - gBlocks; sattn_body(i >> 4, (i >> 2) & 3, i & 3, qkv, so); }
-}
-
-__device__ __forceinline__ void tail_body(
-    int row0, const float* __restrict__ A,
+__device__ __forceinline__ void tail_body(TailSm& sm, int row0, const float* __restrict__ A,
     const float* __restrict__ Wo, const float* __restrict__ bo, const float* __restrict__ res,
     const float* __restrict__ g1, const float* __restrict__ b1n,
     const float* __restrict__ W1, const float* __restrict__ b1f,
@@ -332,13 +288,9 @@
     const float* __restrict__ g2, const float* __restrict__ b2n,
     float* __restrict__ Out)
 {
-  __shared__ float x1[16][132];
-  __shared__ float hid[16][260];
-  __shared__ __align__(16) float sbuf[4352];
-  __shared__ float Sa[32][20];
-  float (*BsA)[136] = (float(*)[136])sbuf;
-  float (*Bs1)[260] = (float(*)[260])sbuf;
-  float (*Bs2)[136] = (float(*)[136])sbuf;
+  float (*BsA)[136] = (float(*)[136])sm.sbuf;
+  float (*Bs1)[260] = (float(*)[260])sm.sbuf;
+  float (*Bs2)[136] = (float(*)[136])sm.sbuf;
   const int tid = threadIdx.x;
   {
     const int tm = tid >> 5, tn = tid & 31;
@@ -348,7 +300,7 @@
     float acc[2][4] = {};
     for (int k0 = 0; k0 < 128; k0 += 32) {
       float2 av = *(const float2*)(A + (size_t)(row0 + ar) * 128 + k0 + ak);
-      Sa[ak][ar] = av.x; Sa[ak + 1][ar] = av.y;
+      sm.Sa[ak][ar] = av.x; sm.Sa[ak + 1][ar] = av.y;
       const float* bp = Wo + (size_t)(k0 + bk) * 128 + be;
       float4 b0v = *(const float4*)(bp + 0);
       float4 b1v = *(const float4*)(bp + 4);
@@ -361,7 +313,7 @@
       __syncthreads();
       #pragma unroll
       for (int kk = 0; kk < 32; kk++) {
-        float2 a = *(const float2*)&Sa[kk][t0];
+        float2 a = *(const float2*)&sm.Sa[kk][t0];
         float4 b = *(const float4*)&BsA[kk][e0];
         acc[0][0] += a.x * b.x; acc[0][1] += a.x * b.y; acc[0][2] += a.x * b.z; acc[0][3] += a.x * b.w;
         acc[1][0] += a.y * b.x; acc[1][1] += a.y * b.y; acc[1][2] += a.y * b.z; acc[1][3] += a.y * b.w;
@@ -384,10 +336,10 @@
       #pragma unroll
       for (int o = 1; o < 32; o <<= 1) sq += __shfl_xor(sq, o);
       float rstd = 1.0f / sqrtf(sq * (1.0f / 128.0f) + 1e-5f);
-      x1[t0 + i][e0 + 0] = d0 * rstd * g1[e0 + 0] + b1n[e0 + 0];
-      x1[t0 + i][e0 + 1] = d1 * rstd * g1[e0 + 1] + b1n[e0 + 1];
-      x1[t0 + i][e0 + 2] = d2 * rstd * g1[e0 + 2] + b1n[e0 + 2];
-      x1[t0 + i][e0 + 3] = d3 * rstd * g1[e0 + 3] + b1n[e0 + 3];
+      sm.x1[t0 + i][e0 + 0] = d0 * rstd * g1[e0 + 0] + b1n[e0 + 0];
+      sm.x1[t0 + i][e0 + 1] = d1 * rstd * g1[e0 + 1] + b1n[e0 + 1];
+      sm.x1[t0 + i][e0 + 2] = d2 * rstd * g1[e0 + 2] + b1n[e0 + 2];
+      sm.x1[t0 + i][e0 + 3] = d3 * rstd * g1[e0 + 3] + b1n[e0 + 3];
     }
   }
   __syncthreads();
@@ -398,7 +350,7 @@
     const int bk = tid >> 4, be = (tid & 15) * 16;
     float acc[4][4] = {};
     for (int k0 = 0; k0 < 128; k0 += 16) {
-      Sa[ak][ar] = x1[ar][k0 + ak];
+      sm.Sa[ak][ar] = sm.x1[ar][k0 + ak];
       const float* bp = W1 + (size_t)(k0 + bk) * 256 + be;
       float4 b0v = *(const float4*)(bp + 0);
       float4 b1v = *(const float4*)(bp + 4);
@@ -411,7 +363,7 @@
       __syncthreads();
       #pragma unroll
       for (int kk = 0; kk < 16; kk++) {
-        float4 a = *(const float4*)&Sa[kk][t0];
+        float4 a = *(const float4*)&sm.Sa[kk][t0];
         float4 b = *(const float4*)&Bs1[kk][e0];
         acc[0][0] += a.x * b.x; acc[0][1] += a.x * b.y; acc[0][2] += a.x * b.z; acc[0][3] += a.x * b.w;
         acc[1][0] += a.y * b.x; acc[1][1] += a.y * b.y; acc[1][2] += a.y * b.z; acc[1][3] += a.y * b.w;
@@ -427,7 +379,7 @@
       hv.y = fmaxf(acc[i][1] + b1f[e0 + 1], 0.0f);
       hv.z = fmaxf(acc[i][2] + b1f[e0 + 2], 0.0f);
       hv.w = fmaxf(acc[i][3] + b1f[e0 + 3], 0.0f);
-      *(float4*)&hid[t0 + i][e0] = hv;
+      *(float4*)&sm.hid[t0 + i][e0] = hv;
     }
   }
   __syncthreads();
@@ -449,8 +401,8 @@
       __syncthreads();
       #pragma unroll
       for (int kk = 0; kk < 32; kk++) {
-        float a0 = hid[t0 + 0][k0 + kk];
-        float a1 = hid[t0 + 1][k0 + kk];
+        float a0 = sm.hid[t0 + 0][k0 + kk];
+        float a1 = sm.hid[t0 + 1][k0 + kk];
         float4 b = *(const float4*)&Bs2[kk][e0];
         acc[0][0] += a0 * b.x; acc[0][1] += a0 * b.y; acc[0][2] += a0 * b.z; acc[0][3] += a0 * b.w;
         acc[1][0] += a1 * b.x; acc[1][1] += a1 * b.y; acc[1][2] += a1 * b.z; acc[1][3] += a1 * b.w;
@@ -460,10 +412,10 @@
     #pragma unroll
     for (int i = 0; i < 2; i++) {
       int r = row0 + t0 + i;
-      float v0 = acc[i][0] + b2f[e0 + 0] + x1[t0 + i][e0 + 0];
-      float v1 = acc[i][1] + b2f[e0 + 1] + x1[t0 + i][e0 + 1];
-      float v2 = acc[i][2] + b2f[e0 + 2] + x1[t0 + i][e0 + 2];
-      float v3 = acc[i][3] + b2f[e0 + 3] + x1[t0 + i][e0 + 3];
+      float v0 = acc[i][0] + b2f[e0 + 0] + sm.x1[t0 + i][e0 + 0];
+      float v1 = acc[i][1] + b2f[e0 + 1] + sm.x1[t0 + i][e0 + 1];
+      float v2 = acc[i][2] + b2f[e0 + 2] + sm.x1[t0 + i][e0 + 2];
+      float v3 = acc[i][3] + b2f[e0 + 3] + sm.x1[t0 + i][e0 + 3];
       float s = v0 + v1 + v2 + v3;
       #pragma unroll
       for (int o = 1; o < 32; o <<= 1) s += __shfl_xor(s, o);
@@ -482,41 +434,114 @@
   }
 }
 
-__global__ __launch_bounds__(256) void tail_k(
-    int gBlocks,
+__device__ __forceinline__ void ln2_body(float* sred4, int r0,
+    const float* __restrict__ x, const float* __restrict__ res,
+    const float* __restrict__ g, const float* __restrict__ b, float* __restrict__ out)
+{
+  const int tid = threadIdx.x;
+  const int e = tid & 127, half = tid >> 7;
+  size_t idx = (size_t)(r0 + half) * 128 + e;
+  float v = x[idx] + res[idx];
+  float s = v;
+  #pragma unroll
+  for (int o = 1; o < 64; o <<= 1) s += __shfl_xor(s, o);
+  if ((tid & 63) == 0) sred4[tid >> 6] = s;
+  __syncthreads();
+  float mean = (sred4[half * 2] + sred4[half * 2 + 1]) * (1.0f / 128.0f);
+  __syncthreads();
+  float d = v - mean;
+  float s2 = d * d;
+  #pragma unroll
+  for (int o = 1; o < 64; o <<= 1) s2 += __shfl_xor(s2, o);
+  if ((tid & 63) == 0) sred4[tid >> 6] = s2;
+  __syncthreads();
+  float var = (sred4[half * 2] + sred4[half * 2 + 1]) * (1.0f / 128.0f);
+  out[idx] = (d / sqrtf(var + 1e-5f)) * g[e] + b[e];
+}
+
+__global__ __launch_bounds__(256) void edge_sqkv_k(
+    int gCount,
+    const float* cea, const float* sea, const int* cei, const int* sei,
+    const float* h, const float* elw, const float* elb, float* aggr,
+    const float* sxs, const float* sw, const float* sb, float* sout)
+{
+  __shared__ K1U u;
+  int bx = blockIdx.x;
+  if (bx < gCount) {
+    edge_body(u.e, bx, cea, sea, cei, sei, h, elw, elb, aggr);
+  } else {
+    int i = bx - gCount;
+    int z = i >> 7, rt = i & 127;
+    gemm16_body(u.g, sxs, sw + z * 128, sb + z * 128, sout + z * 128, rt * 16, 384, 384);
+  }
+}
+
+__global__ __launch_bounds__(256) void ln_sattn_k(
+    int gCount,
+    const float* x, const float* res, const float* g, const float* b, float* out,
+    const float* qkv, float* so)
+{
+  __shared__ K2U u;
+  int bx = blockIdx.x;
+  if (bx < gCount) {
+    ln2_body(u.sred4, bx * 2, x, res, g, b, out);
+  } else {
+    int i = bx - gCount;
+    sattn_body(u.s, i >> 4, (i >> 2) & 3, i & 3, qkv, so);
+  }
+}
+
+__global__ __launch_bounds__(256) void gqkv_stail_k(
+    int gCount,
+    const float* ghb, const float* gqw, const float* gkw, const float* gvw,
+    const float* gqb, const float* gkb, const float* gvb, float* gout,
+    const float* sA, const float* sWo, const float* sbo, const float* sres,
+    const float* sg1, const float* sb1, const float* sW1, const float* sbf1,
+    const float* sW2, const float* sbf2, const float* sg2, const float* sb2, float* sOut)
+{
+  __shared__ K3U u;
+  int bx = blockIdx.x;
+  if (bx < gCount) {
+    int z = bx / 160, rt = bx % 160;
+    const float* B = (z == 0) ? gqw : (z == 1) ? gkw : gvw;
+    const float* bias = (z == 0) ? gqb : (z == 1) ? gkb : gvb;
+    gemm16_body(u.g, ghb, B, bias, gout + (size_t)z * 327680, rt * 16, 128, 128);
+  } else {
+    tail_body(u.t, (bx - gCount) * 16, sA, sWo, sbo, sres, sg1, sb1, sW1, sbf1, sW2, sbf2, sg2, sb2, sOut);
+  }
+}
+
+__global__ __launch_bounds__(256) void gattn_sqkv_k(
+    int gCount,
+    const float* q, const float* k, const float* v, const float* dist, float* go,
+    const float* sxs, const float* sw, const float* sb, float* sout)
+{
+  __shared__ K4U u;
+  int bx = blockIdx.x;
+  if (bx < gCount) {
+    gattn_body(u.a, bx >> 3, bx & 7, q, k, v, dist, go);
+  } else {
+    int i = bx - gCount;
+    int z = i >> 7, rt = i & 127;
+    gemm16_body(u.g, sxs, sw + z * 128, sb + z * 128, sout + z * 128, rt * 16, 384, 384);
+  }
+}
+
+__global__ __launch_bounds__(256) void gtail_sattn_k(
+    int gCount,
     const float* gA, const float* gWo, const float* gbo, const float* gres,
     const float* gg1, const float* gb1, const float* gW1, const float* gbf1,
     const float* gW2, const float* gbf2, const float* gg2, const float* gb2, float* gOut,
-    const float* sA, const float* sWo, const float* sbo, const float* sres,
-    const float* sg1, const float* sb1, const float* sW1, const float* sbf1,
-    const float* sW2, const float* sbf2, const float* sg2, const float* sb2, float* sOut)
-{
+    const float* qkv, float* so)
+{
+  __shared__ K5U u;
   int bx = blockIdx.x;
-  if (bx < gBlocks)
-    tail_body(bx * 16, gA, gWo, gbo, gres, gg1, gb1, gW1, gbf1, gW2, gbf2, gg2, gb2, gOut);
-  else
-    tail_body((bx - gBlocks) * 16, sA, sWo, sbo, sres, sg1, sb1, sW1, sbf1, sW2, sbf2, sg2, sb2, sOut);
-}
-
-__global__ __launch_bounds__(128) void ln_k(
-    const float* __restrict__ x, const float* __restrict__ res,
-    const float* __restrict__ g, const float* __restrict__ b, float* __restrict__ out)
-{
-  __shared__ float sred[2];
-  int r = blockIdx.x, e = threadIdx.x;
-  size_t idx = (size_t)r * 128 + e;
-  float v = x[idx] + res[idx];
-  float nv = blk_norm(v, e, sred);
-  out[idx] = nv * g[e] + b[e];
-}
-
-__global__ __launch_bounds__(128) void embed_k(
-    const int* __restrict__ tokens, const float* __restrict__ tok_emb,
-    const float* __restrict__ pos_emb, float* __restrict__ xs)
-{
-  int r = blockIdx.x, e = threadIdx.x;
-  int tk = tokens[r];
-  xs[(size_t)r * 128 + e] = tok_emb[(size_t)tk * 128 + e] + pos_emb[(size_t)(r & 127) * 128 + e];
+  if (bx < gCount) {
+    tail_body(u.t, bx * 16, gA, gWo, gbo, gres, gg1, gb1, gW1, gbf1, gW2, gbf2, gg2, gb2, gOut);
+  } else {
+    int i = bx - gCount;
+    sattn_body(u.s, i >> 4, (i >> 2) & 3, i & 3, qkv, so);
+  }
 }
 
 __global__ __launch_bounds__(128) void head_k(
@@ -573,8 +598,25 @@
     __syncthreads();
     a = ob[e];
     for (int f = 0; f < 128; f++) a += t1[f] * ow[f * 128 + e];
-    float nv = blk_norm(G[e] + a, e, sred);
-    G[e] = nv * n1g[l * 128 + e] + n1b[l * 128 + e];
+    float v = G[e] + a;
+    {
+      float s = v;
+      #pragma unroll
+      for (int o = 1; o < 64; o <<= 1) s += __shfl_xor(s, o);
+      if ((e & 63) == 0) sred[e >> 6] = s;
+      __syncthreads();
+      float mean = (sred[0] + sred[1]) * (1.0f / 128.0f);
+      __syncthreads();
+      float d = v - mean;
+      float s2 = d * d;
+      #pragma unroll
+      for (int o = 1; o < 64; o <<= 1) s2 += __shfl_xor(s2, o);
+      if ((e & 63) == 0) sred[e >> 6] = s2;
+      __syncthreads();
+      float var = (sred[0] + sred[1]) * (1.0f / 128.0f);
+      __syncthreads();
+      G[e] = (d / sqrtf(var + 1e-5f)) * n1g[l * 128 + e] + n1b[l * 128 + e];
+    }
     __syncthreads();
     const float* vw2 = s2g_vw + (size_t)l * 16384; const float* vb2 = s2g_vb + l * 128;
     const float* ow2 = s2g_ow + (size_t)l * 16384; const float* ob2 = s2g_ob + l * 128;
@@ -584,8 +626,25 @@
     __syncthreads();
     a = ob2[e];
     for (int f = 0; f < 128; f++) a += t1[f] * ow2[f * 128 + e];
-    nv = blk_norm(Sm[e] + a, e, sred);
-    Sm[e] = nv * n2g[l * 128 + e] + n2b[l * 128 + e];
+    float v2x = Sm[e] + a;
+    {
+      float s = v2x;
+      #pragma unroll
+      for (int o = 1; o < 64; o <<= 1) s += __shfl_xor(s, o);
+      if ((e & 63) == 0) sred[e >> 6] = s;
+      __syncthreads();
+      float mean = (sred[0] + sred[1]) * (1.0f / 128.0f);
+      __syncthreads();
+      float d = v2x - mean;
+      float s2 = d * d;
+      #pragma unroll
+      for (int o = 1; o < 64; o <<= 1) s2 += __shfl_xor(s2, o);
+      if ((e & 63) == 0) sred[e >> 6] = s2;
+      __syncthreads();
+      float var = (sred[0] + sred[1]) * (1.0f / 128.0f);
+      __syncthreads();
+      Sm[e] = (d / sqrtf(var + 1e-5f)) * n2g[l * 128 + e] + n2b[l * 128 + e];
+    }
     __syncthreads();
   }
   t2[e] = 0.5f * (G[e] + Sm[e]);
@@ -692,36 +751,42 @@
   float* satto = alloc(2048 * 128);
   float* xsfin = alloc(2048 * 128);
 
-  node_proj_k<<<2560, 128, 0, stream>>>(conf_x, scaf_x, gproj_w, gproj_b, h, aggr);
-  dist_k<<<80, 256, 0, stream>>>(conf_pos, scaf_pos, distb);
-  edge_gemm_k<<<dim3(160, 7), 256, 0, stream>>>(conf_ea, scaf_ea, conf_ei, scaf_ei, h, elin_w, elin_b, aggr);
-  ln_k<<<2560, 128, 0, stream>>>(aggr, h, eln_g, eln_b, hb);
-  embed_k<<<2048, 128, 0, stream>>>(tokens, tok_emb, pos_emb, xs2);
-
-  for (int l = 0; l < 4; l++) {
-    const bool hasG = (l < 3);
-    const int lg = hasG ? l : 0;
-    const int gq = hasG ? 480 : 0;
-    const int ga = hasG ? 640 : 0;
-    const int gt = hasG ? 160 : 0;
-    float* sOut = (l == 3) ? xsfin : xs2;
-    qkv_k<<<gq + 384, 256, 0, stream>>>(gq,
-        hb, gt_qw + (size_t)lg * 16384, gt_kw + (size_t)lg * 16384, gt_vw + (size_t)lg * 16384,
-        gt_qb + lg * 128, gt_kb + lg * 128, gt_vb + lg * 128, qb,
-        xs2, se_inw + (size_t)l * 49152, se_inb + l * 384, qkv3);
-    attn_k<<<ga + 256, 256, 0, stream>>>(ga, qb, qb + 327680, qb + 655360, distb, atto, qkv3, satto);
-    tail_k<<<gt + 128, 256, 0, stream>>>(gt,
-        atto, gt_ow + (size_t)lg * 16384, gt_ob + lg * 128, hb,
-        gt_ln1g + lg * 128, gt_ln1b + lg * 128,
-        gt_f1w + (size_t)lg * 32768, gt_f1b + lg * 256,
-        gt_f2w + (size_t)lg * 32768, gt_f2b + lg * 128,
-        gt_ln2g + lg * 128, gt_ln2b + lg * 128, hb,
+  front_k<<<2384, 256, 0, stream>>>(conf_x, scaf_x, gproj_w, gproj_b, h, aggr,
+                                    conf_pos, scaf_pos, distb,
+                                    tokens, tok_emb, pos_emb, xs2);
+  edge_sqkv_k<<<1504, 256, 0, stream>>>(1120,
+      conf_ea, scaf_ea, conf_ei, scaf_ei, h, elin_w, elin_b, aggr,
+      xs2, se_inw, se_inb, qkv3);
+  ln_sattn_k<<<1536, 256, 0, stream>>>(1280, aggr, h, eln_g, eln_b, hb, qkv3, satto);
+
+  for (int l = 0; l < 3; l++) {
+    gqkv_stail_k<<<608, 256, 0, stream>>>(480,
+        hb, gt_qw + (size_t)l * 16384, gt_kw + (size_t)l * 16384, gt_vw + (size_t)l * 16384,
+        gt_qb + l * 128, gt_kb + l * 128, gt_vb + l * 128, qb,
         satto, se_ow + (size_t)l * 16384, se_ob + l * 128, xs2,
         se_ln1g + l * 128, se_ln1b + l * 128,
         se_f1w + (size_t)l * 32768, se_f1b + l * 256,
         se_f2w + (size_t)l * 32768, se_f2b + l * 128,
-        se_ln2g + l * 128, se_ln2b + l * 128, sOut);
-  }
+        se_ln2g + l * 128, se_ln2b + l * 128, xs2);
+    gattn_sqkv_k<<<1024, 256, 0, stream>>>(640,
+        qb, qb + 327680, qb + 655360, distb, atto,
+        xs2, se_inw + (size_t)(l + 1) * 49152, se_inb + (l + 1) * 384, qkv3);
+    gtail_sattn_k<<<416, 256, 0, stream>>>(160,
+        atto, gt_ow + (size_t)l * 16384, gt_ob + l * 128, hb,
+        gt_ln1g + l * 128, gt_ln1b + l * 128,
+        gt_f1w + (size_t)l * 32768, gt_f1b + l * 256,
+        gt_f2w + (size_t)l * 32768, gt_f2b + l * 128,
+        gt_ln2g + l * 128, gt_ln2b + l * 128, hb,
+        qkv3, satto);
+  }
+
+  gqkv_stail_k<<<128, 256, 0, stream>>>(0,
+      hb, gt_qw, gt_kw, gt_vw, gt_qb, gt_kb, gt_vb, qb,
+      satto, se_ow + (size_t)3 * 16384, se_ob + 3 * 128, xs2,
+      se_ln1g + 3 * 128, se_ln1b + 3 * 128,
+      se_f1w + (size_t)3 * 32768, se_f1b + 3 * 256,
+      se_f2w + (size_t)3 * 32768, se_f2b + 3 * 128,
+      se_ln2g + 3 * 128, se_ln2b + 3 * 128, xsfin);
 
   head_k<<<16, 128, 0, stream>>>(hb, xsfin, gfeat,
                                  fg1_w, fg1_b, fg2_w, fg2_b,
```

New measurement: 676.9 us. +2.0%, slower.
